# Performance work log

Hardware: AMD Instinct MI355X
Metric: run time of the kernel (lower is better)

The kernel has to match this reference:

```python
import jax, jax.numpy as jnp
import numpy as np


def setup_inputs() -> dict:
    key = jax.random.key(0)
    k1, k2 = jax.random.split(key)
    num_classes, queries_per_class, prototypes_per_class, embedding_dim = 19, 5, 5, 1024
    batch = 1024
    num_queries = num_classes * queries_per_class  # 95
    query_features = jax.random.normal(k1, (batch, num_queries, embedding_dim), dtype=jnp.float32)
    # nn.Embedding default init: N(0,1)
    weight = jax.random.normal(k2, (num_classes * (prototypes_per_class + 1), embedding_dim), dtype=jnp.float32)
    return {
        "query_features": query_features,
        "weight": weight,
        "num_classes": num_classes,
        "queries_per_class": queries_per_class,
        "prototypes_per_class": prototypes_per_class,
    }


def reference(query_features, weight, num_classes, queries_per_class, prototypes_per_class):
    B, Q, D = query_features.shape
    P = prototypes_per_class
    # class index for each query: [Q]
    class_indices = jnp.repeat(jnp.arange(num_classes), queries_per_class)
    # prototype row indices per query: [Q, P+1]
    proto_indices = class_indices[:, None] * (P + 1) + jnp.arange(P + 1)[None, :]
    # gathered prototypes: [Q, P+1, D] (shared across batch; no batch expansion)
    proto = weight[proto_indices]
    # positive sims against the P class prototypes: [B, Q, P]
    pos_sim = jnp.einsum("bqd,qkd->bqk", query_features, proto[:, :P, :])
    # background sim against last embedding: [B, Q]
    bg_sim = jnp.einsum("bqd,qd->bq", query_features, proto[:, P, :])
    pos_max = jnp.max(pos_sim, axis=-1)  # [B, Q]
    logits = jnp.full((B, Q, num_classes + 1), -jnp.inf, dtype=query_features.dtype)
    logits = logits.at[:, jnp.arange(Q), class_indices].set(pos_max)
    logits = logits.at[:, :, -1].set(bg_sim)
    return logits
```

## Files before the change

kernel.cpp:

```cpp
#include <hip/hip_runtime.h>
#include <math.h>
#include <float.h>


typedef float f32x4 __attribute__((ext_vector_type(4)));

#define NB 4
#define NEG_FILL (-3.0e38f)

template <int DD>
__global__ __launch_bounds__(256) void codebook_head_kernel(
    const float* __restrict__ qf,
    const float* __restrict__ w,
    float* __restrict__ out,
    int B, int Q,
    int num_classes, int qpc, int P)
{
    const int wave_id = (blockIdx.x * blockDim.x + threadIdx.x) >> 6;
    const int lane    = threadIdx.x & 63;
    const int bblocks = (B + NB - 1) / NB;
    const int total   = bblocks * Q;
    if (wave_id >= total) return;

    const int q   = wave_id % Q;
    const int b0  = (wave_id / Q) * NB;
    const int cls = q / qpc;

    const float* proto = w + (size_t)cls * (P + 1) * DD;

    float acc[6][NB];
#pragma unroll
    for (int k = 0; k < 6; ++k)
#pragma unroll
        for (int j = 0; j < NB; ++j)
            acc[k][j] = 0.f;

#pragma unroll
    for (int d0 = 0; d0 < DD; d0 += 64 * 4) {
        const int d = d0 + lane * 4;

        f32x4 pv[6];
#pragma unroll
        for (int k = 0; k < 6; ++k)
            pv[k] = *reinterpret_cast<const f32x4*>(proto + (size_t)k * DD + d);

#pragma unroll
        for (int j = 0; j < NB; ++j) {
            const int bj = (b0 + j < B) ? (b0 + j) : (B - 1);
            const f32x4 qv = __builtin_nontemporal_load(
                reinterpret_cast<const f32x4*>(qf + ((size_t)bj * Q + q) * DD + d));
#pragma unroll
            for (int k = 0; k < 6; ++k)
                acc[k][j] += qv.x * pv[k].x + qv.y * pv[k].y +
                             qv.z * pv[k].z + qv.w * pv[k].w;
        }
    }

#pragma unroll
    for (int k = 0; k < 6; ++k) {
#pragma unroll
        for (int j = 0; j < NB; ++j) {
            float v = acc[k][j];
#pragma unroll
            for (int off = 32; off > 0; off >>= 1)
                v += __shfl_xor(v, off);
            acc[k][j] = v;
        }
    }

#pragma unroll
    for (int j = 0; j < NB; ++j) {
        if (b0 + j >= B) break;
        const float pos_max = fmaxf(fmaxf(fmaxf(acc[0][j], acc[1][j]),
                                          fmaxf(acc[2][j], acc[3][j])), acc[4][j]);
        const float bg = acc[5][j];
        float* orow = out + ((size_t)(b0 + j) * Q + q) * (num_classes + 1);
        if (lane < num_classes + 1) {
            float v = NEG_FILL;
            if (lane == cls)         v = pos_max;
            if (lane == num_classes) v = bg;
            __builtin_nontemporal_store(v, orow + lane);
        }
    }
}

__global__ __launch_bounds__(256) void codebook_head_kernel_gen(
    const float* __restrict__ qf, const float* __restrict__ w,
    float* __restrict__ out, int B, int Q, int D,
    int num_classes, int qpc, int P)
{
    const int wave_id = (blockIdx.x * blockDim.x + threadIdx.x) >> 6;
    const int lane    = threadIdx.x & 63;
    const int bblocks = (B + NB - 1) / NB;
    if (wave_id >= bblocks * Q) return;
    const int q = wave_id % Q, b0 = (wave_id / Q) * NB, cls = q / qpc;
    const float* proto = w + (size_t)cls * (P + 1) * D;
    float acc[6][NB];
    for (int k = 0; k < 6; ++k)
        for (int j = 0; j < NB; ++j) acc[k][j] = 0.f;
    for (int d = lane * 4; d < D; d += 256) {
        f32x4 pv[6];
        for (int k = 0; k < 6; ++k)
            pv[k] = *reinterpret_cast<const f32x4*>(proto + (size_t)k * D + d);
        for (int j = 0; j < NB; ++j) {
            const int bj = (b0 + j < B) ? (b0 + j) : (B - 1);
            const f32x4 qv = *reinterpret_cast<const f32x4*>(qf + ((size_t)bj * Q + q) * D + d);
            for (int k = 0; k < 6; ++k)
                acc[k][j] += qv.x * pv[k].x + qv.y * pv[k].y + qv.z * pv[k].z + qv.w * pv[k].w;
        }
    }
    for (int k = 0; k < 6; ++k)
        for (int j = 0; j < NB; ++j) {
            float v = acc[k][j];
            for (int off = 32; off > 0; off >>= 1) v += __shfl_xor(v, off);
            acc[k][j] = v;
        }
    for (int j = 0; j < NB; ++j) {
        if (b0 + j >= B) break;
        const float pos_max = fmaxf(fmaxf(fmaxf(acc[0][j], acc[1][j]),
                                          fmaxf(acc[2][j], acc[3][j])), acc[4][j]);
        const float bg = acc[5][j];
        float* orow = out + ((size_t)(b0 + j) * Q + q) * (num_classes + 1);
        if (lane < num_classes + 1) {
            float v = NEG_FILL;
            if (lane == cls)         v = pos_max;
            if (lane == num_classes) v = bg;
            orow[lane] = v;
        }
    }
}

extern "C" void kernel_launch(void* const* d_in, const int* in_sizes, int n_in,
                              void* d_out, int out_size, void* d_ws, size_t ws_size,
                              hipStream_t stream)
{
    const float* qf = (const float*)d_in[0];
    const float* w  = (const float*)d_in[1];
    float* out = (float*)d_out;

    const int num_classes = 19;
    const int qpc         = 5;
    const int P           = 5;
    const int rows        = num_classes * (P + 1);
    const int D           = in_sizes[1] / rows;
    const int Q           = num_classes * qpc;
    const int B           = in_sizes[0] / (Q * D);

    const int bblocks = (B + NB - 1) / NB;
    const int total_waves = bblocks * Q;
    const int waves_per_block = 4;
    const int blocks = (total_waves + waves_per_block - 1) / waves_per_block;

    if (D == 1024) {
        codebook_head_kernel<1024><<<blocks, waves_per_block * 64, 0, stream>>>(
            qf, w, out, B, Q, num_classes, qpc, P);
    } else {
        codebook_head_kernel_gen<<<blocks, waves_per_block * 64, 0, stream>>>(
            qf, w, out, B, Q, D, num_classes, qpc, P);
    }
}
```

Measured before the change: 87.14 us.

## Stream queries per wave with register-cached prototypes and prefetched query rows

Each wave now handles one batch row and a contiguous segment of about 12 queries. It keeps the six prototype rows for the current class in registers, reloading them only when the class changes, and software-prefetches the next query row while computing the current one. Output rows are written as 5 float4 stores instead of 20 scalar stores. The aim is to cut redundant prototype loads and hide memory latency, at the cost of far more registers (96 floats of prototypes plus double-buffered queries), which may lower occupancy.

```diff
diff --git a/kernel.cpp b/kernel.cpp
--- a/kernel.cpp
+++ b/kernel.cpp
@@ -5,85 +5,101 @@
 
 typedef float f32x4 __attribute__((ext_vector_type(4)));
 
-#define NB 4
 #define NEG_FILL (-3.0e38f)
 
-template <int DD>
-__global__ __launch_bounds__(256) void codebook_head_kernel(
+__global__ __launch_bounds__(256) void codebook_stream(
     const float* __restrict__ qf,
     const float* __restrict__ w,
     float* __restrict__ out,
-    int B, int Q,
-    int num_classes, int qpc, int P)
+    int B, int Q, int NC, int qpc, int nseg, int qpw)
 {
+    const int lane    = threadIdx.x & 63;
     const int wave_id = (blockIdx.x * blockDim.x + threadIdx.x) >> 6;
-    const int lane    = threadIdx.x & 63;
-    const int bblocks = (B + NB - 1) / NB;
-    const int total   = bblocks * Q;
+    const int total   = B * nseg;
     if (wave_id >= total) return;
 
-    const int q   = wave_id % Q;
-    const int b0  = (wave_id / Q) * NB;
-    const int cls = q / qpc;
+    const int b  = wave_id % B;
+    const int q0 = (wave_id / B) * qpw;
+    const int q1 = (q0 + qpw < Q) ? (q0 + qpw) : Q;
+    if (q0 >= Q) return;
 
-    const float* proto = w + (size_t)cls * (P + 1) * DD;
+    const int doff = lane * 4;
+    const float* qbase = qf + (size_t)b * Q * 1024 + doff;
 
-    float acc[6][NB];
+    f32x4 qv[4], qn[4];
 #pragma unroll
-    for (int k = 0; k < 6; ++k)
+    for (int c = 0; c < 4; ++c)
+        qv[c] = __builtin_nontemporal_load(
+            reinterpret_cast<const f32x4*>(qbase + (size_t)q0 * 1024 + c * 256));
+
+    f32x4 pv[6][4];
+    int cur_cls = -1;
+
+    for (int q = q0; q < q1; ++q) {
+        const bool have_next = (q + 1 < q1);
+        if (have_next) {
 #pragma unroll
-        for (int j = 0; j < NB; ++j)
-            acc[k][j] = 0.f;
+            for (int c = 0; c < 4; ++c)
+                qn[c] = __builtin_nontemporal_load(
+                    reinterpret_cast<const f32x4*>(qbase + (size_t)(q + 1) * 1024 + c * 256));
+        }
+
+        const int cls = q / qpc;
+        if (cls != cur_cls) {
+            cur_cls = cls;
+            const float* proto = w + (size_t)cls * 6 * 1024 + doff;
+#pragma unroll
+            for (int k = 0; k < 6; ++k)
+#pragma unroll
+                for (int c = 0; c < 4; ++c)
+                    pv[k][c] = *reinterpret_cast<const f32x4*>(
+                        proto + (size_t)k * 1024 + c * 256);
+        }
+
+        float acc[6] = {0.f, 0.f, 0.f, 0.f, 0.f, 0.f};
+#pragma unroll
+        for (int c = 0; c < 4; ++c) {
+#pragma unroll
+            for (int k = 0; k < 6; ++k)
+                acc[k] += qv[c].x * pv[k][c].x + qv[c].y * pv[k][c].y +
+                          qv[c].z * pv[k][c].z + qv[c].w * pv[k][c].w;
+        }
 
 #pragma unroll
-    for (int d0 = 0; d0 < DD; d0 += 64 * 4) {
-        const int d = d0 + lane * 4;
-
-        f32x4 pv[6];
-#pragma unroll
-        for (int k = 0; k < 6; ++k)
-            pv[k] = *reinterpret_cast<const f32x4*>(proto + (size_t)k * DD + d);
-
-#pragma unroll
-        for (int j = 0; j < NB; ++j) {
-            const int bj = (b0 + j < B) ? (b0 + j) : (B - 1);
-            const f32x4 qv = __builtin_nontemporal_load(
-                reinterpret_cast<const f32x4*>(qf + ((size_t)bj * Q + q) * DD + d));
-#pragma unroll
-            for (int k = 0; k < 6; ++k)
-                acc[k][j] += qv.x * pv[k].x + qv.y * pv[k].y +
-                             qv.z * pv[k].z + qv.w * pv[k].w;
-        }
-    }
-
-#pragma unroll
-    for (int k = 0; k < 6; ++k) {
-#pragma unroll
-        for (int j = 0; j < NB; ++j) {
-            float v = acc[k][j];
+        for (int k = 0; k < 6; ++k) {
+            float v = acc[k];
 #pragma unroll
             for (int off = 32; off > 0; off >>= 1)
                 v += __shfl_xor(v, off);
-            acc[k][j] = v;
+            acc[k] = v;
         }
-    }
 
+        const float pm = fmaxf(fmaxf(fmaxf(acc[0], acc[1]),
+                                     fmaxf(acc[2], acc[3])), acc[4]);
+        const float bg = acc[5];
+
+        if (lane < 5) {
+            f32x4 v;
 #pragma unroll
-    for (int j = 0; j < NB; ++j) {
-        if (b0 + j >= B) break;
-        const float pos_max = fmaxf(fmaxf(fmaxf(acc[0][j], acc[1][j]),
-                                          fmaxf(acc[2][j], acc[3][j])), acc[4][j]);
-        const float bg = acc[5][j];
-        float* orow = out + ((size_t)(b0 + j) * Q + q) * (num_classes + 1);
-        if (lane < num_classes + 1) {
-            float v = NEG_FILL;
-            if (lane == cls)         v = pos_max;
-            if (lane == num_classes) v = bg;
-            __builtin_nontemporal_store(v, orow + lane);
+            for (int t = 0; t < 4; ++t) {
+                const int c = lane * 4 + t;
+                float x = NEG_FILL;
+                if (c == cls) x = pm;
+                if (c == NC)  x = bg;
+                v[t] = x;
+            }
+            __builtin_nontemporal_store(v,
+                reinterpret_cast<f32x4*>(out + ((size_t)b * Q + q) * (NC + 1) + lane * 4));
+        }
+
+        if (have_next) {
+#pragma unroll
+            for (int c = 0; c < 4; ++c) qv[c] = qn[c];
         }
     }
 }
 
+#define NB 4
 __global__ __launch_bounds__(256) void codebook_head_kernel_gen(
     const float* __restrict__ qf, const float* __restrict__ w,
     float* __restrict__ out, int B, int Q, int D,
@@ -106,7 +122,8 @@
             const int bj = (b0 + j < B) ? (b0 + j) : (B - 1);
             const f32x4 qv = *reinterpret_cast<const f32x4*>(qf + ((size_t)bj * Q + q) * D + d);
             for (int k = 0; k < 6; ++k)
-                acc[k][j] += qv.x * pv[k].x + qv.y * pv[k].y + qv.z * pv[k].z + qv.w * pv[k].w;
+                acc[k][j] += qv.x * pv[k].x + qv.y * pv[k].y +
+                             qv.z * pv[k].z + qv.w * pv[k].w;
         }
     }
     for (int k = 0; k < 6; ++k)
@@ -146,16 +163,18 @@
     const int Q           = num_classes * qpc;
     const int B           = in_sizes[0] / (Q * D);
 
-    const int bblocks = (B + NB - 1) / NB;
-    const int total_waves = bblocks * Q;
-    const int waves_per_block = 4;
-    const int blocks = (total_waves + waves_per_block - 1) / waves_per_block;
-
-    if (D == 1024) {
-        codebook_head_kernel<1024><<<blocks, waves_per_block * 64, 0, stream>>>(
-            qf, w, out, B, Q, num_classes, qpc, P);
+    if (D == 1024 && P == 5) {
+        const int nseg = 8;
+        const int qpw  = (Q + nseg - 1) / nseg;
+        const int total_waves = B * nseg;
+        const int blocks = (total_waves + 3) / 4;
+        codebook_stream<<<blocks, 256, 0, stream>>>(
+            qf, w, out, B, Q, num_classes, qpc, nseg, qpw);
     } else {
-        codebook_head_kernel_gen<<<blocks, waves_per_block * 64, 0, stream>>>(
+        const int bblocks = (B + NB - 1) / NB;
+        const int total_waves = bblocks * Q;
+        const int blocks = (total_waves + 3) / 4;
+        codebook_head_kernel_gen<<<blocks, 256, 0, stream>>>(
             qf, w, out, B, Q, D, num_classes, qpc, P);
     }
 }
```

New measurement: 99.18 us. +13.8%, slower.
